# Kernel optimization log

Measured on AMD Instinct MI355X. Metric: run time of the kernel, lower is better.

## Reference

```python
import jax, jax.numpy as jnp
import numpy as np

MU = 0.75
H = W = 256


def _bending_energy_one(pred):
    """pred: (2, 256, 256) probabilities. Returns scalar bending energy."""
    mask = (pred[1] > 0.5).astype(jnp.float32)  # (H, W) binary nucleus mask
    p = jnp.pad(mask, 1)
    # 8-neighbor count (3x3 ones kernel with zero center)
    nc = (p[:-2, :-2] + p[:-2, 1:-1] + p[:-2, 2:] +
          p[1:-1, :-2] + p[1:-1, 2:] +
          p[2:, :-2] + p[2:, 1:-1] + p[2:, 2:])
    contour = (mask == 1.0) & (nc < 8.0)  # (H, W) bool
    flat = contour.reshape(-1)            # (H*W,)
    N = flat.shape[0]
    # Stable argsort puts contour pixel indices first, in ascending
    # (row-major) order == torch.nonzero ordering. Fixed output shape.
    order = jnp.argsort(~flat, stable=True)  # (N,) int
    m = flat.sum()                            # number of contour points
    rows = (order // W).astype(jnp.float32)
    cols = (order % W).astype(jnp.float32)
    pts = jnp.stack([rows, cols], axis=-1)    # (N, 2)

    v1 = pts[1:-1] - pts[:-2]   # point - prev_point, centers 1..N-2
    v2 = pts[2:] - pts[1:-1]    # next_point - point
    cross = v1[:, 0] * v2[:, 1] - v1[:, 1] * v2[:, 0]
    dot = (v1 * v2).sum(-1)
    n1 = jnp.sqrt((v1 ** 2).sum(-1))
    n2 = jnp.sqrt((v2 ** 2).sum(-1))
    curv = jnp.where(cross == 0.0, 0.0,
                     2.0 * jnp.abs(cross) / (n1 * n2 + dot))
    delta = jnp.where(cross >= 0.0, 0.0, 1.0)
    be = (1.0 - delta + delta * MU) * curv ** 2 / (n1 + n2)
    # valid centers are indices 1..m-2 of the contour list -> j <= m-3
    j = jnp.arange(N - 2)
    valid = j <= (m - 3)
    return jnp.where(valid, be, 0.0).sum()


def setup_inputs() -> dict:
    key = jax.random.key(0)
    k1, k2 = jax.random.split(key)
    B = 128
    inp = jax.random.normal(k1, (B, 2, H, W), dtype=jnp.float32)
    tgt = jax.random.uniform(k2, (B, 2, H, W), dtype=jnp.float32)
    return {"input": inp, "target": tgt}


def reference(input, target):
    per_image = jax.vmap(_bending_energy_one)(target)  # (B,)
    return per_image.sum() / input.shape[0]
```

## Files before the change

kernel.cpp:

```cpp
#include <hip/hip_runtime.h>

#define NWORDS 1024

__device__ __forceinline__ int next_set(const unsigned long long* cw, int pos) {
    int w = pos >> 6;
    int b = pos & 63;
    unsigned long long m = cw[w];
    m = (b == 63) ? 0ULL : (m & (~0ULL << (b + 1)));
    while (m == 0ULL) {
        ++w;
        if (w >= NWORDS) return -1;
        m = cw[w];
    }
    return (w << 6) + __builtin_ctzll(m);
}

__global__ __launch_bounds__(1024)
void bending_loss_kernel(const float* __restrict__ target, float* __restrict__ out,
                         float inv_b) {
#pragma clang fp contract(off)
    __shared__ unsigned long long bits[NWORDS];
    __shared__ unsigned long long cw[NWORDS];
    __shared__ float wsum[16];

    const int img_idx = blockIdx.x;
    const int tid  = threadIdx.x;
    const int wave = tid >> 6;
    const int lane = tid & 63;

    const float* img = target + (size_t)img_idx * 131072 + 65536;

    for (int k = wave; k < NWORDS; k += 16) {
        float v = img[(k << 6) + lane];
        unsigned long long bal = __ballot(v > 0.5f);
        if (lane == 0) bits[k] = bal;
    }
    __syncthreads();

    {
        const int k = tid;
        const int r = k >> 2, wp = k & 3;
        auto get = [&](int rr, int ww) -> unsigned long long {
            return (rr < 0 || rr > 255 || ww < 0 || ww > 3)
                       ? 0ULL : bits[(rr << 2) + ww];
        };
        unsigned long long A  = get(r - 1, wp);
        unsigned long long C  = bits[k];
        unsigned long long B  = get(r + 1, wp);
        unsigned long long Ap = get(r - 1, wp - 1), An = get(r - 1, wp + 1);
        unsigned long long Cp = get(r,     wp - 1), Cn = get(r,     wp + 1);
        unsigned long long Bp = get(r + 1, wp - 1), Bn = get(r + 1, wp + 1);
        unsigned long long interior =
            ((A << 1) | (Ap >> 63)) & A & ((A >> 1) | (An << 63)) &
            ((C << 1) | (Cp >> 63)) &     ((C >> 1) | (Cn << 63)) &
            ((B << 1) | (Bp >> 63)) & B & ((B >> 1) | (Bn << 63));
        cw[k] = C & ~interior;
    }
    __syncthreads();

    float sum = 0.0f;
    {
        unsigned long long my = cw[tid];
        if (my) {
            int p0 = (tid << 6) + __builtin_ctzll(my);
            const int lim = (tid + 1) << 6;
            int p1 = next_set(cw, p0);
            int p2 = (p1 >= 0) ? next_set(cw, p1) : -1;
            while (p0 < lim && p2 >= 0) {
                float r0 = (float)(p0 >> 8), c0 = (float)(p0 & 255);
                float r1 = (float)(p1 >> 8), c1 = (float)(p1 & 255);
                float r2 = (float)(p2 >> 8), c2 = (float)(p2 & 255);
                float v1r = r1 - r0, v1c = c1 - c0;
                float v2r = r2 - r1, v2c = c2 - c1;
                float cross = v1r * v2c - v1c * v2r;
                if (cross != 0.0f) {
                    float dot = v1r * v2r + v1c * v2c;
                    float n1 = sqrtf(v1r * v1r + v1c * v1c);
                    float n2 = sqrtf(v2r * v2r + v2c * v2c);
                    float curv = (2.0f * fabsf(cross)) / (n1 * n2 + dot);
                    float factor = (cross >= 0.0f) ? 1.0f : 0.75f;
                    sum += (factor * (curv * curv)) / (n1 + n2);
                }
                p0 = p1; p1 = p2;
                p2 = next_set(cw, p2);
            }
        }
    }

    for (int off = 32; off > 0; off >>= 1) sum += __shfl_down(sum, off);
    if (lane == 0) wsum[wave] = sum;
    __syncthreads();
    if (tid == 0) {
        float t = 0.0f;
        for (int i = 0; i < 16; ++i) t += wsum[i];
        atomicAdd(out, t * inv_b);
    }
}

extern "C" void kernel_launch(void* const* d_in, const int* in_sizes, int n_in,
                              void* d_out, int out_size, void* d_ws, size_t ws_size,
                              hipStream_t stream) {
    const float* target = (const float*)d_in[1];
    float* out = (float*)d_out;
    const int B = in_sizes[1] / (2 * 256 * 256);

    hipMemsetAsync(out, 0, sizeof(float) * out_size, stream);
    bending_loss_kernel<<<dim3(B), dim3(1024), 0, stream>>>(target, out, 1.0f / (float)B);
}
```

Baseline: 157.2 us.

## Split into band-parallel contour build and byte-chunked energy kernels

```diff
diff --git a/kernel.cpp b/kernel.cpp
--- a/kernel.cpp
+++ b/kernel.cpp
@@ -1,6 +1,9 @@
 #include <hip/hip_runtime.h>
 
-#define NWORDS 1024
+#define NW 1024
+#define BANDROWS 32
+#define NBANDS 8
+#define NSEG 8
 
 __device__ __forceinline__ int next_set(const unsigned long long* cw, int pos) {
     int w = pos >> 6;
@@ -9,81 +12,98 @@
     m = (b == 63) ? 0ULL : (m & (~0ULL << (b + 1)));
     while (m == 0ULL) {
         ++w;
-        if (w >= NWORDS) return -1;
+        if (w >= NW) return -1;
         m = cw[w];
     }
     return (w << 6) + __builtin_ctzll(m);
 }
 
 __global__ __launch_bounds__(1024)
-void bending_loss_kernel(const float* __restrict__ target, float* __restrict__ out,
-                         float inv_b) {
-#pragma clang fp contract(off)
-    __shared__ unsigned long long bits[NWORDS];
-    __shared__ unsigned long long cw[NWORDS];
-    __shared__ float wsum[16];
+void contour_build_kernel(const float* __restrict__ target,
+                          unsigned long long* __restrict__ cwg) {
+    __shared__ unsigned long long lb[(BANDROWS + 2) * 4];
 
-    const int img_idx = blockIdx.x;
+    const int img  = blockIdx.x;
+    const int band = blockIdx.y;
     const int tid  = threadIdx.x;
-    const int wave = tid >> 6;
-    const int lane = tid & 63;
+    const int wave = tid >> 6, lane = tid & 63;
 
-    const float* img = target + (size_t)img_idx * 131072 + 65536;
+    const float* imgp = target + (size_t)img * 131072 + 65536;
+    const int r0 = band * BANDROWS - 1;
 
-    for (int k = wave; k < NWORDS; k += 16) {
-        float v = img[(k << 6) + lane];
-        unsigned long long bal = __ballot(v > 0.5f);
-        if (lane == 0) bits[k] = bal;
+    for (int w = wave; w < (BANDROWS + 2) * 4; w += 16) {
+        const int gr = r0 + (w >> 2);
+        unsigned long long bal = 0ULL;
+        if (gr >= 0 && gr <= 255) {
+            float v = imgp[(gr << 8) + ((w & 3) << 6) + lane];
+            bal = __ballot(v > 0.5f);
+        }
+        if (lane == 0) lb[w] = bal;
     }
     __syncthreads();
 
-    {
-        const int k = tid;
-        const int r = k >> 2, wp = k & 3;
+    if (tid < BANDROWS * 4) {
+        const int k  = tid;
+        const int lr = 1 + (k >> 2);
+        const int wp = k & 3;
         auto get = [&](int rr, int ww) -> unsigned long long {
-            return (rr < 0 || rr > 255 || ww < 0 || ww > 3)
-                       ? 0ULL : bits[(rr << 2) + ww];
+            return (ww < 0 || ww > 3) ? 0ULL : lb[(rr << 2) + ww];
         };
-        unsigned long long A  = get(r - 1, wp);
-        unsigned long long C  = bits[k];
-        unsigned long long B  = get(r + 1, wp);
-        unsigned long long Ap = get(r - 1, wp - 1), An = get(r - 1, wp + 1);
-        unsigned long long Cp = get(r,     wp - 1), Cn = get(r,     wp + 1);
-        unsigned long long Bp = get(r + 1, wp - 1), Bn = get(r + 1, wp + 1);
+        unsigned long long A  = get(lr - 1, wp);
+        unsigned long long C  = lb[(lr << 2) + wp];
+        unsigned long long Bx = get(lr + 1, wp);
+        unsigned long long Ap = get(lr - 1, wp - 1), An = get(lr - 1, wp + 1);
+        unsigned long long Cp = get(lr,     wp - 1), Cn = get(lr,     wp + 1);
+        unsigned long long Bp = get(lr + 1, wp - 1), Bn = get(lr + 1, wp + 1);
         unsigned long long interior =
-            ((A << 1) | (Ap >> 63)) & A & ((A >> 1) | (An << 63)) &
-            ((C << 1) | (Cp >> 63)) &     ((C >> 1) | (Cn << 63)) &
-            ((B << 1) | (Bp >> 63)) & B & ((B >> 1) | (Bn << 63));
-        cw[k] = C & ~interior;
+            ((A  << 1) | (Ap >> 63)) & A  & ((A  >> 1) | (An << 63)) &
+            ((C  << 1) | (Cp >> 63)) &      ((C  >> 1) | (Cn << 63)) &
+            ((Bx << 1) | (Bp >> 63)) & Bx & ((Bx >> 1) | (Bn << 63));
+        cwg[(size_t)img * NW + band * (BANDROWS * 4) + k] = C & ~interior;
     }
+}
+
+__global__ __launch_bounds__(1024)
+void bending_energy_kernel(const unsigned long long* __restrict__ cwg,
+                           float* __restrict__ out, float inv_b) {
+#pragma clang fp contract(off)
+    __shared__ unsigned long long cw[NW];
+    __shared__ float wsum[16];
+
+    const int img = blockIdx.x;
+    const int seg = blockIdx.y;
+    const int tid = threadIdx.x;
+    const int wave = tid >> 6, lane = tid & 63;
+
+    cw[tid] = cwg[(size_t)img * NW + tid];
     __syncthreads();
 
     float sum = 0.0f;
-    {
-        unsigned long long my = cw[tid];
-        if (my) {
-            int p0 = (tid << 6) + __builtin_ctzll(my);
-            const int lim = (tid + 1) << 6;
-            int p1 = next_set(cw, p0);
-            int p2 = (p1 >= 0) ? next_set(cw, p1) : -1;
-            while (p0 < lim && p2 >= 0) {
-                float r0 = (float)(p0 >> 8), c0 = (float)(p0 & 255);
-                float r1 = (float)(p1 >> 8), c1 = (float)(p1 & 255);
-                float r2 = (float)(p2 >> 8), c2 = (float)(p2 & 255);
-                float v1r = r1 - r0, v1c = c1 - c0;
-                float v2r = r2 - r1, v2c = c2 - c1;
-                float cross = v1r * v2c - v1c * v2r;
-                if (cross != 0.0f) {
-                    float dot = v1r * v2r + v1c * v2c;
-                    float n1 = sqrtf(v1r * v1r + v1c * v1c);
-                    float n2 = sqrtf(v2r * v2r + v2c * v2c);
-                    float curv = (2.0f * fabsf(cross)) / (n1 * n2 + dot);
-                    float factor = (cross >= 0.0f) ? 1.0f : 0.75f;
-                    sum += (factor * (curv * curv)) / (n1 + n2);
-                }
-                p0 = p1; p1 = p2;
-                p2 = next_set(cw, p2);
+    const int chunk = seg * 1024 + tid;
+    const int word = chunk >> 3, sh = (chunk & 7) << 3;
+    const unsigned int byte = (unsigned int)((cw[word] >> sh) & 0xFFULL);
+    if (byte) {
+        int p0 = (chunk << 3) + __builtin_ctz(byte);
+        const int lim = (chunk + 1) << 3;
+        int p1 = next_set(cw, p0);
+        int p2 = (p1 >= 0) ? next_set(cw, p1) : -1;
+        while (p0 < lim && p2 >= 0) {
+            float r0f = (float)(p0 >> 8), c0f = (float)(p0 & 255);
+            float r1f = (float)(p1 >> 8), c1f = (float)(p1 & 255);
+            float r2f = (float)(p2 >> 8), c2f = (float)(p2 & 255);
+            float v1r = r1f - r0f, v1c = c1f - c0f;
+            float v2r = r2f - r1f, v2c = c2f - c1f;
+            float cross = v1r * v2c - v1c * v2r;
+            if (cross != 0.0f) {
+                float dot = v1r * v2r + v1c * v2c;
+                float n1 = sqrtf(v1r * v1r + v1c * v1c);
+                float n2 = sqrtf(v2r * v2r + v2c * v2c);
+                float curv = (2.0f * fabsf(cross)) / (n1 * n2 + dot);
+                float factor = (cross >= 0.0f) ? 1.0f : 0.75f;
+                sum += (factor * (curv * curv)) / (n1 + n2);
             }
+            p0 = p1; p1 = p2;
+            p2 = next_set(cw, p2);
         }
     }
 
@@ -103,7 +123,9 @@
     const float* target = (const float*)d_in[1];
     float* out = (float*)d_out;
     const int B = in_sizes[1] / (2 * 256 * 256);
+    unsigned long long* cwg = (unsigned long long*)d_ws;
 
     hipMemsetAsync(out, 0, sizeof(float) * out_size, stream);
-    bending_loss_kernel<<<dim3(B), dim3(1024), 0, stream>>>(target, out, 1.0f / (float)B);
+    contour_build_kernel<<<dim3(B, NBANDS), dim3(1024), 0, stream>>>(target, cwg);
+    bending_energy_kernel<<<dim3(B, NSEG), dim3(1024), 0, stream>>>(cwg, out, 1.0f / (float)B);
 }
```

Measured after the change: 151.0 us. 4.0% less time.
